# Optimization experiments

Hardware: AMD Instinct MI355X
Metric: run time of the kernel (lower is better)

The kernel has to match this reference:

```python
import jax, jax.numpy as jnp
import numpy as np

N, G, HID, LAT, E_RAND = 20000, 3000, 256, 32, 320000
EPS = 1e-8
NEG_SLOPE = 0.2  # PyG GATv2Conv default leaky_relu slope


def _segment_softmax(logits, seg, n):
    # numerically stable softmax over edges grouped by destination node
    m = jax.ops.segment_max(logits, seg, num_segments=n)
    ex = jnp.exp(logits - m[seg])
    s = jax.ops.segment_sum(ex, seg, num_segments=n)
    return ex / (s[seg] + 1e-16)


def _gatv2(x, src, dst, Wl, Wr, att, b, n):
    # GATv2 (heads=1): score = att . leaky_relu(Wl x_j + Wr x_i)
    xl = x @ Wl  # [N, C] source transform (also the message)
    xr = x @ Wr  # [N, C] destination transform
    e = jax.nn.leaky_relu(xl[src] + xr[dst], NEG_SLOPE)  # [E, C]
    logit = e @ att  # [E]
    alpha = _segment_softmax(logit, dst, n)
    out = jax.ops.segment_sum(alpha[:, None] * xl[src], dst, num_segments=n)
    return out + b


def _log_zinb(x, mu, theta, pi):
    theta = theta[None, :]
    softplus_pi = jax.nn.softplus(-pi)
    log_theta_eps = jnp.log(theta + EPS)
    log_theta_mu_eps = jnp.log(theta + mu + EPS)
    pi_theta_log = -pi + theta * (log_theta_eps - log_theta_mu_eps)
    case_zero = jax.nn.softplus(pi_theta_log) - softplus_pi
    case_nz = (-softplus_pi + pi_theta_log
               + x * (jnp.log(mu + EPS) - log_theta_mu_eps)
               + jax.lax.lgamma(x + theta) - jax.lax.lgamma(theta)
               - jax.lax.lgamma(x + 1.0))
    return jnp.where(x < EPS, case_zero, 0.0) + jnp.where(x > EPS, case_nz, 0.0)


def setup_inputs():
    key = jax.random.key(0)
    ks = jax.random.split(key, 14)
    x = jax.random.randint(ks[0], (N, G), 0, 20).astype(jnp.float32)
    er = jax.random.randint(ks[1], (2, E_RAND), 0, N, dtype=jnp.int32)
    loops = jnp.tile(jnp.arange(N, dtype=jnp.int32)[None, :], (2, 1))
    edge_index = jnp.concatenate([er, loops], axis=1)  # [2, 340000] incl self-loops
    noise = jax.random.normal(ks[2], (N, LAT), dtype=jnp.float32)

    def init(k, shape, fan_in):
        return jax.random.normal(k, shape, dtype=jnp.float32) / np.float32(np.sqrt(fan_in))

    Wl1 = init(ks[3], (G, HID), G); Wr1 = init(ks[4], (G, HID), G)
    att1 = init(ks[5], (HID,), HID); b1 = jnp.zeros((HID,), jnp.float32)
    Wl2 = init(ks[6], (HID, 2 * LAT), HID); Wr2 = init(ks[7], (HID, 2 * LAT), HID)
    att2 = init(ks[8], (2 * LAT,), 2 * LAT); b2 = jnp.zeros((2 * LAT,), jnp.float32)
    Wd1 = init(ks[9], (LAT, HID), LAT); bd1 = jnp.zeros((HID,), jnp.float32)
    Wd2 = init(ks[10], (HID, G), HID); bd2 = jnp.zeros((G,), jnp.float32)
    Wdo = init(ks[11], (HID, G), HID); bdo = jnp.zeros((G,), jnp.float32)
    theta = jax.random.uniform(ks[12], (G,), minval=0.5, maxval=2.0, dtype=jnp.float32)
    return dict(x=x, edge_index=edge_index, noise=noise,
                Wl1=Wl1, Wr1=Wr1, att1=att1, b1=b1,
                Wl2=Wl2, Wr2=Wr2, att2=att2, b2=b2,
                Wd1=Wd1, bd1=bd1, Wd2=Wd2, bd2=bd2, Wdo=Wdo, bdo=bdo,
                theta=theta)


def reference(x, edge_index, noise, Wl1, Wr1, att1, b1, Wl2, Wr2, att2, b2,
              Wd1, bd1, Wd2, bd2, Wdo, bdo, theta):
    n = x.shape[0]
    src, dst = edge_index[0], edge_index[1]
    # --- GATv2 encoder ---
    h = _gatv2(x, src, dst, Wl1, Wr1, att1, b1, n)
    h2 = _gatv2(jax.nn.relu(h), src, dst, Wl2, Wr2, att2, b2, n)  # [N, 2*LAT]
    mu_z, logvar = h2[:, :LAT], h2[:, LAT:]
    # --- reparameterize: std = sqrt(exp(logvar)) ---
    z = mu_z + noise * jnp.exp(0.5 * logvar)
    # --- ZINB decoder ---
    hd = z @ Wd1 + bd1
    mean = jax.nn.softplus(hd @ Wd2 + bd2)
    pi = hd @ Wdo + bdo
    # --- loss: -E[log ZINB] + KL(q(z|x) || N(0,I)) ---
    recon = -jnp.mean(jnp.sum(_log_zinb(x, mean, theta, pi), axis=1))
    kl = jnp.mean(0.5 * jnp.sum(mu_z ** 2 + jnp.exp(logvar) - logvar - 1.0, axis=1))
    return recon + kl
```

## Files before the change

kernel.cpp:

```cpp
#include <hip/hip_runtime.h>
#include <math.h>

#define NN   20000
#define GG   3000
#define HIDD 256
#define LATT 32
#define FEPS 1e-8f

typedef __attribute__((ext_vector_type(8))) __bf16 bf16x8;
typedef __attribute__((ext_vector_type(4))) float f32x4;

__device__ __forceinline__ float fsp(float v) {
    float t = __expf(-fabsf(v));
    return fmaxf(v, 0.f) + __logf(1.f + t);
}
__device__ __forceinline__ float sp_approx(float t) {
    float a = fabsf(t);
    float den = fmaf(a, fmaf(a, fmaf(a, 0.8382f, -1.4958f), 1.87f), 1.f);
    return fmaxf(t, 0.f) + 0.6931472f * __builtin_amdgcn_rcpf(den);
}
__device__ __forceinline__ float lrelu(float v) {
    return v > 0.f ? v : 0.2f * v;
}
__device__ __forceinline__ ushort f2bf(float f) {
    uint b = __float_as_uint(f);
    return (ushort)((b + 0x7FFFu + ((b >> 16) & 1u)) >> 16);
}

__global__ void zinb_table(const float* __restrict__ theta, float* __restrict__ tabL,
                           float* __restrict__ logte, int G_) {
    int idx = blockIdx.x * blockDim.x + threadIdx.x;
    if (idx >= G_ * 20) return;
    int g = idx / 20, c = idx % 20;
    float th = theta[g];
    tabL[idx] = lgammaf((float)c + th) - lgammaf(th) - lgammaf((float)c + 1.f);
    if (c == 0) logte[g] = logf(th + FEPS);
}

__global__ void edge_hist(const int* __restrict__ ei, int* __restrict__ cnt, int E) {
    int e = blockIdx.x * blockDim.x + threadIdx.x;
    if (e < E) atomicAdd(&cnt[ei[E + e]], 1);
}

__global__ __launch_bounds__(1024)
void scan_deg(int* __restrict__ cnt_cur, int* __restrict__ rowptr, int Nn) {
    __shared__ int ts[1024];
    int t = threadIdx.x;
    int chunk = (Nn + 1023) / 1024;
    int beg = t * chunk, end = min(beg + chunk, Nn);
    int s = 0;
    for (int i = beg; i < end; i++) s += cnt_cur[i];
    ts[t] = s;
    __syncthreads();
    for (int off = 1; off < 1024; off <<= 1) {
        int v = (t >= off) ? ts[t - off] : 0;
        __syncthreads();
        ts[t] += v;
        __syncthreads();
    }
    int run = (t == 0) ? 0 : ts[t - 1];
    for (int i = beg; i < end; i++) {
        int c = cnt_cur[i];
        rowptr[i] = run;
        cnt_cur[i] = run;
        run += c;
    }
    if (t == 1023) rowptr[Nn] = ts[1023];
}

__global__ void edge_scatter(const int* __restrict__ ei, int* __restrict__ cur,
                             int* __restrict__ eidx, int E) {
    int e = blockIdx.x * blockDim.x + threadIdx.x;
    if (e < E) {
        int p = atomicAdd(&cur[ei[E + e]], 1);
        eidx[p] = e;
    }
}

__global__ __launch_bounds__(256)
void transp_bf16(const float* __restrict__ in, ushort* __restrict__ out, int K, int N) {
    __shared__ ushort t[32][33];
    int k0 = blockIdx.x * 32, n0 = blockIdx.y * 32;
    int tx = threadIdx.x & 31, ty = threadIdx.x >> 5;
    #pragma unroll
    for (int u = 0; u < 32; u += 8) {
        int k = k0 + ty + u, n = n0 + tx;
        t[ty + u][tx] = (k < K && n < N) ? f2bf(in[(size_t)k * N + n]) : (ushort)0;
    }
    __syncthreads();
    #pragma unroll
    for (int u = 0; u < 32; u += 8) {
        int n = n0 + ty + u, k = k0 + tx;
        if (n < N && k < K) out[(size_t)n * K + k] = t[tx][ty + u];
    }
}

template<bool ABF, bool ZEP>
__global__ __launch_bounds__(256, 4)
void mfma_dual(const void* __restrict__ Ap, const ushort* __restrict__ B1t,
               const ushort* __restrict__ B2t, float* __restrict__ C1,
               float* __restrict__ C2, const float* __restrict__ xg,
               const float* __restrict__ tabL, const float* __restrict__ theta,
               const float* __restrict__ logte, const float* __restrict__ bd2,
               const float* __restrict__ bdo, double* __restrict__ partsR,
               int M, int K, int Nc) {
    __shared__ __align__(16) char lds[ZEP ? 32768 : 24576];
    char* ldsA  = lds;
    char* ldsB1 = lds + 8192;
    char* ldsB2 = lds + 16384;
    char* xsb   = lds + 24576;
    __shared__ float thetas[ZEP ? 64 : 1], thltes[ZEP ? 64 : 1];
    __shared__ float bd2s[ZEP ? 64 : 1], bdos[ZEP ? 64 : 1];
    __shared__ float tabs[ZEP ? 64 * 20 : 1];
    __shared__ double redd[4];

    const int tid = threadIdx.x;
    const int nwg = gridDim.x * gridDim.y;
    const int orig = blockIdx.y * gridDim.x + blockIdx.x;
    const int q = nwg >> 3, r = nwg & 7, xcd = orig & 7;
    const int vv = (xcd < r ? xcd * (q + 1) : r * (q + 1) + (xcd - r) * q) + (orig >> 3);
    const int bx = vv % gridDim.x, by = vv / gridDim.x;
    const int m0 = by * 64, n0 = bx * 64;
    const int lane = tid & 63, wid = tid >> 6;
    const int wr = wid >> 1, wc = wid & 1;
    const int frow = lane & 15;
    const int fkb = (lane >> 4) << 4;

    if (ZEP) {
        #pragma unroll
        for (int u = 0; u < 2; u++) {
            int c = tid + (u << 8);
            int row = c >> 3, col8 = (c & 7) << 3;
            int gm = m0 + row, gn = n0 + col8;
            uint4 w = make_uint4(0u, 0u, 0u, 0u);
            if (gm < M && gn < Nc) {
                const float* af = xg + (size_t)gm * Nc + gn;
                float4 lo = *(const float4*)af;
                float4 hi = *(const float4*)(af + 4);
                w.x = (uint)f2bf(lo.x) | ((uint)f2bf(lo.y) << 16);
                w.y = (uint)f2bf(lo.z) | ((uint)f2bf(lo.w) << 16);
                w.z = (uint)f2bf(hi.x) | ((uint)f2bf(hi.y) << 16);
                w.w = (uint)f2bf(hi.z) | ((uint)f2bf(hi.w) << 16);
            }
            int o = (row << 7) + (col8 << 1);
            o ^= (row & 7) << 4;
            *(uint4*)(xsb + o) = w;
        }
        for (int i = tid; i < 64; i += 256) {
            int g = n0 + i;
            bool ok = g < Nc;
            float th = ok ? theta[g] : 1.f;
            thetas[i] = th;
            thltes[i] = ok ? th * logte[g] : 0.f;
            bd2s[i]   = ok ? bd2[g]   : 0.f;
            bdos[i]   = ok ? bdo[g]   : 0.f;
        }
        for (int i = tid; i < 64 * 20; i += 256) {
            int g = n0 + i / 20;
            tabs[i] = (g < Nc) ? tabL[(size_t)g * 20 + i % 20] : 0.f;
        }
    }

    f32x4 acc1[2][2], acc2[2][2];
    #pragma unroll
    for (int i = 0; i < 2; i++)
        #pragma unroll
        for (int j = 0; j < 2; j++) {
            acc1[i][j] = (f32x4){0.f, 0.f, 0.f, 0.f};
            acc2[i][j] = (f32x4){0.f, 0.f, 0.f, 0.f};
        }

    const int nk = (K + 63) >> 6;
    for (int t = 0; t < nk; t++) {
        const int k0 = t << 6;
        #pragma unroll
        for (int u = 0; u < 2; u++) {
            int c = tid + (u << 8);
            int row = c >> 3, col8 = (c & 7) << 3;
            int gm = m0 + row, gk = k0 + col8;
            uint4 w = make_uint4(0u, 0u, 0u, 0u);
            if (gm < M && gk < K) {
                if (ABF) {
                    w = *(const uint4*)((const ushort*)Ap + (size_t)gm * K + gk);
                } else {
                    const float* af = (const float*)Ap + (size_t)gm * K + gk;
                    float4 lo = *(const float4*)af;
                    float4 hi = *(const float4*)(af + 4);
                    w.x = (uint)f2bf(lo.x) | ((uint)f2bf(lo.y) << 16);
                    w.y = (uint)f2bf(lo.z) | ((uint)f2bf(lo.w) << 16);
                    w.z = (uint)f2bf(hi.x) | ((uint)f2bf(hi.y) << 16);
                    w.w = (uint)f2bf(hi.z) | ((uint)f2bf(hi.w) << 16);
                }
            }
            int o = (row << 7) + (col8 << 1);
            o ^= (row & 7) << 4;
            *(uint4*)(ldsA + o) = w;
        }
        #pragma unroll
        for (int u = 0; u < 2; u++) {
            int c = tid + (u << 8);
            int row = c >> 3, col8 = (c & 7) << 3;
            int gn = n0 + row, gk = k0 + col8;
            uint4 w1 = make_uint4(0u, 0u, 0u, 0u), w2 = w1;
            if (gn < Nc && gk < K) {
                size_t o = (size_t)gn * K + gk;
                w1 = *(const uint4*)(B1t + o);
                w2 = *(const uint4*)(B2t + o);
            }
            int o = (row << 7) + (col8 << 1);
            o ^= (row & 7) << 4;
            *(uint4*)(ldsB1 + o) = w1;
            *(uint4*)(ldsB2 + o) = w2;
        }
        __syncthreads();
        #pragma unroll
        for (int kk = 0; kk < 2; kk++) {
            int kb = (kk << 6) + fkb;
            bf16x8 af[2], b1f[2], b2f[2];
            #pragma unroll
            for (int mi = 0; mi < 2; mi++) {
                int rr = (wr << 5) + (mi << 4) + frow;
                int o = ((rr << 7) + kb) ^ ((rr & 7) << 4);
                af[mi] = *(const bf16x8*)(ldsA + o);
            }
            #pragma unroll
            for (int ni = 0; ni < 2; ni++) {
                int rr = (wc << 5) + (ni << 4) + frow;
                int o = ((rr << 7) + kb) ^ ((rr & 7) << 4);
                b1f[ni] = *(const bf16x8*)(ldsB1 + o);
                b2f[ni] = *(const bf16x8*)(ldsB2 + o);
            }
            #pragma unroll
            for (int mi = 0; mi < 2; mi++)
                #pragma unroll
                for (int ni = 0; ni < 2; ni++) {
                    acc1[mi][ni] = __builtin_amdgcn_mfma_f32_16x16x32_bf16(af[mi], b1f[ni], acc1[mi][ni], 0, 0, 0);
                    acc2[mi][ni] = __builtin_amdgcn_mfma_f32_16x16x32_bf16(af[mi], b2f[ni], acc2[mi][ni], 0, 0, 0);
                }
        }
        __syncthreads();
    }

    const int lr = (lane >> 4) << 2;
    if (!ZEP) {
        #pragma unroll
        for (int mi = 0; mi < 2; mi++)
            #pragma unroll
            for (int ni = 0; ni < 2; ni++) {
                int gmb = m0 + (wr << 5) + (mi << 4) + lr;
                int gn  = n0 + (wc << 5) + (ni << 4) + frow;
                if (gn >= Nc) continue;
                f32x4 v1 = acc1[mi][ni], v2 = acc2[mi][ni];
                #pragma unroll
                for (int j = 0; j < 4; j++) {
                    int gm = gmb + j;
                    if (gm < M) {
                        C1[(size_t)gm * Nc + gn] = v1[j];
                        C2[(size_t)gm * Nc + gn] = v2[j];
                    }
                }
            }
    } else {
        float lsum = 0.f;
        #pragma unroll
        for (int mi = 0; mi < 2; mi++)
            #pragma unroll
            for (int ni = 0; ni < 2; ni++) {
                int lcol = (wc << 5) + (ni << 4) + frow;
                int gn = n0 + lcol;
                int lrow0 = (wr << 5) + (mi << 4) + lr;
                if (gn >= Nc) continue;
                f32x4 am = acc1[mi][ni], ap = acc2[mi][ni];
                float th = thetas[lcol], thlte = thltes[lcol];
                float bm = bd2s[lcol], bp = bdos[lcol];
                #pragma unroll
                for (int j = 0; j < 4; j++) {
                    int lrow = lrow0 + j;
                    if (m0 + lrow >= M) continue;
                    float mu  = fsp(am[j] + bm);
                    float pi  = ap[j] + bp;
                    float spp = fsp(pi);
                    float ltme = __logf(th + mu + FEPS);
                    float lmu  = __logf(mu + FEPS);
                    int o = (lrow << 7) + (lcol << 1);
                    o ^= (lrow & 7) << 4;
                    ushort ub = *(const ushort*)(xsb + o);
                    float xv = __uint_as_float((uint)ub << 16);
                    int xi = (int)(xv + 0.5f);
                    float ptl = fmaf(-th, ltme, thlte) - pi;
                    float corr = (xv < FEPS) ? sp_approx(-ptl) : 0.f;
                    float term = thlte + tabs[lcol * 20 + xi] - spp
                               - (th + xv) * ltme + xv * lmu + corr;
                    lsum += term;
                }
            }
        #pragma unroll
        for (int off = 32; off; off >>= 1) lsum += __shfl_down(lsum, off);
        if (lane == 0) redd[wid] = (double)lsum;
        __syncthreads();
        if (tid == 0)
            partsR[by * gridDim.x + bx] = redd[0] + redd[1] + redd[2] + redd[3];
    }
}

template<int DW, int OM>
__global__ __launch_bounds__(256)
void gat_attn(const float* __restrict__ xl, const float* __restrict__ xr,
              const float* __restrict__ att, const int* __restrict__ ei,
              const int* __restrict__ rowptr, const int* __restrict__ eidx,
              const float* __restrict__ bias, void* __restrict__ out,
              int D, int Nn) {
    __shared__ float lbuf[4][64];
    int wid = threadIdx.x >> 6, lane = threadIdx.x & 63;
    int n = blockIdx.x * 4 + wid;
    if (n >= Nn) return;
    int k = lane * DW;
    float xrr[DW], ats[DW], hacc[DW];
    if (DW == 4) {
        float4 a4 = *(const float4*)(att + k);
        float4 r4 = *(const float4*)(xr + (size_t)n * D + k);
        ats[0] = a4.x; ats[1] = a4.y; ats[2] = a4.z; ats[3] = a4.w;
        xrr[0] = r4.x; xrr[1] = r4.y; xrr[2] = r4.z; xrr[3] = r4.w;
    } else {
        ats[0] = att[k];
        xrr[0] = xr[(size_t)n * D + k];
    }
    #pragma unroll
    for (int d = 0; d < DW; d++) hacc[d] = 0.f;
    float m = -3.0e38f, ssum = 0.f;
    int beg = rowptr[n], end = rowptr[n + 1];
    for (int c0 = beg; c0 < end; c0 += 64) {
        int cnt = min(64, end - c0);
        for (int j = 0; j < cnt; j++) {
            int e = eidx[c0 + j];
            const float* xs = xl + (size_t)ei[e] * D + k;
            float p;
            if (DW == 4) {
                float4 v = *(const float4*)xs;
                p = ats[0] * lrelu(v.x + xrr[0]) + ats[1] * lrelu(v.y + xrr[1])
                  + ats[2] * lrelu(v.z + xrr[2]) + ats[3] * lrelu(v.w + xrr[3]);
            } else {
                p = ats[0] * lrelu(xs[0] + xrr[0]);
            }
            #pragma unroll
            for (int o2 = 32; o2; o2 >>= 1) p += __shfl_down(p, o2);
            if (lane == 0) lbuf[wid][j] = p;
        }
        float cm = (lane < cnt) ? lbuf[wid][lane] : -3.0e38f;
        #pragma unroll
        for (int o2 = 32; o2; o2 >>= 1) cm = fmaxf(cm, __shfl_xor(cm, o2));
        float mnew = fmaxf(m, cm);
        float scale = __expf(m - mnew);
        ssum *= scale;
        #pragma unroll
        for (int d = 0; d < DW; d++) hacc[d] *= scale;
        for (int j = 0; j < cnt; j++) {
            int e = eidx[c0 + j];
            float w = __expf(lbuf[wid][j] - mnew);
            ssum += w;
            const float* xs = xl + (size_t)ei[e] * D + k;
            if (DW == 4) {
                float4 v = *(const float4*)xs;
                hacc[0] = fmaf(w, v.x, hacc[0]);
                hacc[1] = fmaf(w, v.y, hacc[1]);
                hacc[2] = fmaf(w, v.z, hacc[2]);
                hacc[3] = fmaf(w, v.w, hacc[3]);
            } else {
                hacc[0] = fmaf(w, xs[0], hacc[0]);
            }
        }
        m = mnew;
    }
    float inv = 1.f / (ssum + 1e-16f);
    if (DW == 4) {
        float4 b = *(const float4*)(bias + k);
        float r0 = fmaf(hacc[0], inv, b.x), r1 = fmaf(hacc[1], inv, b.y);
        float r2 = fmaf(hacc[2], inv, b.z), r3 = fmaf(hacc[3], inv, b.w);
        if (OM == 0) {
            *(float4*)((float*)out + (size_t)n * D + k) = make_float4(r0, r1, r2, r3);
        } else {
            ushort4 o;
            o.x = f2bf(fmaxf(r0, 0.f)); o.y = f2bf(fmaxf(r1, 0.f));
            o.z = f2bf(fmaxf(r2, 0.f)); o.w = f2bf(fmaxf(r3, 0.f));
            *(ushort4*)((ushort*)out + (size_t)n * D + k) = o;
        }
    } else {
        float r0 = fmaf(hacc[0], inv, bias[k]);
        if (OM == 0) ((float*)out)[(size_t)n * D + k] = r0;
        else         ((ushort*)out)[(size_t)n * D + k] = f2bf(fmaxf(r0, 0.f));
    }
}

__global__ __launch_bounds__(256)
void z_kl(const float* __restrict__ h2, const float* __restrict__ noise,
          float* __restrict__ z, double* __restrict__ partsK, int Nn) {
    __shared__ double rd[4];
    int gid = blockIdx.x * blockDim.x + threadIdx.x;
    int n = gid >> 5, k = gid & 31;
    float kt = 0.f;
    if (n < Nn) {
        float mu = h2[(size_t)n * 64 + k];
        float lv = h2[(size_t)n * 64 + 32 + k];
        float ev = expf(lv);
        z[(size_t)n * 32 + k] = mu + noise[(size_t)n * 32 + k] * expf(0.5f * lv);
        kt = 0.5f * (mu * mu + ev - lv - 1.f);
    }
    #pragma unroll
    for (int off = 32; off; off >>= 1) kt += __shfl_down(kt, off);
    int wid = threadIdx.x >> 6, lane = threadIdx.x & 63;
    if (lane == 0) rd[wid] = (double)kt;
    __syncthreads();
    if (threadIdx.x == 0) partsK[blockIdx.x] = rd[0] + rd[1] + rd[2] + rd[3];
}

__global__ __launch_bounds__(256)
void hd_gemm(const float* __restrict__ z, const float* __restrict__ Wd1,
             const float* __restrict__ bd1, ushort* __restrict__ hd, int Nn) {
    __shared__ float Ws[32 * 256];
    __shared__ float zs[32 * 32];
    int tid = threadIdx.x;
    #pragma unroll
    for (int i = 0; i < 32; i++) Ws[i * 256 + tid] = Wd1[i * 256 + tid];
    int r0 = blockIdx.x * 32;
    for (int i = tid; i < 32 * 32; i += 256) {
        int r = i >> 5, c = i & 31;
        zs[i] = (r0 + r < Nn) ? z[(size_t)(r0 + r) * 32 + c] : 0.f;
    }
    __syncthreads();
    float b = bd1[tid];
    for (int r = 0; r < 32; r++) {
        if (r0 + r >= Nn) break;
        float acc = b;
        #pragma unroll
        for (int k2 = 0; k2 < 32; k2++) acc = fmaf(zs[r * 32 + k2], Ws[k2 * 256 + tid], acc);
        hd[(size_t)(r0 + r) * 256 + tid] = f2bf(acc);
    }
}

__global__ __launch_bounds__(256)
void final_reduce(const double* __restrict__ pR, int nR,
                  const double* __restrict__ pK, int nK,
                  float* __restrict__ out, int Nn) {
    __shared__ double sd[256];
    double s = 0.0;
    for (int i = threadIdx.x; i < nR; i += 256) s -= pR[i];
    for (int i = threadIdx.x; i < nK; i += 256) s += pK[i];
    sd[threadIdx.x] = s;
    __syncthreads();
    for (int o = 128; o; o >>= 1) {
        if (threadIdx.x < o) sd[threadIdx.x] += sd[threadIdx.x + o];
        __syncthreads();
    }
    if (threadIdx.x == 0) out[0] = (float)(sd[0] / (double)Nn);
}

extern "C" void kernel_launch(void* const* d_in, const int* in_sizes, int n_in,
                              void* d_out, int out_size, void* d_ws, size_t ws_size,
                              hipStream_t stream) {
    const int N_ = NN, G_ = GG, HID_ = HIDD;
    const float* x     = (const float*)d_in[0];
    const int*   ei    = (const int*)d_in[1];
    const float* noise = (const float*)d_in[2];
    const float* Wl1   = (const float*)d_in[3];
    const float* Wr1   = (const float*)d_in[4];
    const float* att1  = (const float*)d_in[5];
    const float* b1    = (const float*)d_in[6];
    const float* Wl2   = (const float*)d_in[7];
    const float* Wr2   = (const float*)d_in[8];
    const float* att2  = (const float*)d_in[9];
    const float* b2    = (const float*)d_in[10];
    const float* Wd1   = (const float*)d_in[11];
    const float* bd1   = (const float*)d_in[12];
    const float* Wd2   = (const float*)d_in[13];
    const float* bd2   = (const float*)d_in[14];
    const float* Wdo   = (const float*)d_in[15];
    const float* bdo   = (const float*)d_in[16];
    const float* theta = (const float*)d_in[17];
    const int E = in_sizes[1] / 2;

    const int MB = (N_ + 63) / 64;
    const int dgx = (G_ + 63) / 64;
    const int nR = dgx * MB;
    const int nKb = (N_ * 32) / 256;

    char* base = (char*)d_ws;
    size_t off = 0;
    auto alloc = [&](size_t bytes) -> char* {
        char* p = base + off;
        off = (off + bytes + 255) & ~(size_t)255;
        return p;
    };
    double* partsR = (double*)alloc((size_t)nR * 8);
    double* partsK = (double*)alloc((size_t)nKb * 8);
    float*  tabL  = (float*)alloc((size_t)G_ * 20 * 4);
    float*  logte = (float*)alloc((size_t)G_ * 4);
    int*    rowptr= (int*)alloc((size_t)(N_ + 1) * 4);
    int*    cur   = (int*)alloc((size_t)N_ * 4);
    int*    eidx  = (int*)alloc((size_t)E * 4);
    ushort* Wl1t  = (ushort*)alloc((size_t)HID_ * G_ * 2);
    ushort* Wr1t  = (ushort*)alloc((size_t)HID_ * G_ * 2);
    ushort* Wl2t  = (ushort*)alloc((size_t)64 * HID_ * 2);
    ushort* Wr2t  = (ushort*)alloc((size_t)64 * HID_ * 2);
    ushort* Wd2t  = (ushort*)alloc((size_t)G_ * HID_ * 2);
    ushort* Wdot  = (ushort*)alloc((size_t)G_ * HID_ * 2);
    float*  xl1   = (float*)alloc((size_t)N_ * HID_ * 4);
    float*  xr1   = (float*)alloc((size_t)N_ * HID_ * 4);
    ushort* h_bf  = (ushort*)alloc((size_t)N_ * HID_ * 2);
    float*  xl2   = (float*)alloc((size_t)N_ * 64 * 4);
    float*  xr2   = (float*)alloc((size_t)N_ * 64 * 4);
    float*  h2    = (float*)alloc((size_t)N_ * 64 * 4);
    float*  zb    = (float*)alloc((size_t)N_ * 32 * 4);

    ushort* hdb = (ushort*)xr1;
    float*  outf = (float*)d_out;

    hipMemsetAsync(cur, 0, N_ * sizeof(int), stream);

    zinb_table<<<(G_ * 20 + 255) / 256, 256, 0, stream>>>(theta, tabL, logte, G_);
    edge_hist<<<(E + 255) / 256, 256, 0, stream>>>(ei, cur, E);
    scan_deg<<<1, 1024, 0, stream>>>(cur, rowptr, N_);
    edge_scatter<<<(E + 255) / 256, 256, 0, stream>>>(ei, cur, eidx, E);

    transp_bf16<<<dim3((G_ + 31) / 32, (HID_ + 31) / 32), 256, 0, stream>>>(Wl1, Wl1t, G_, HID_);
    transp_bf16<<<dim3((G_ + 31) / 32, (HID_ + 31) / 32), 256, 0, stream>>>(Wr1, Wr1t, G_, HID_);
    transp_bf16<<<dim3((HID_ + 31) / 32, 2), 256, 0, stream>>>(Wl2, Wl2t, HID_, 64);
    transp_bf16<<<dim3((HID_ + 31) / 32, 2), 256, 0, stream>>>(Wr2, Wr2t, HID_, 64);
    transp_bf16<<<dim3((HID_ + 31) / 32, (G_ + 31) / 32), 256, 0, stream>>>(Wd2, Wd2t, HID_, G_);
    transp_bf16<<<dim3((HID_ + 31) / 32, (G_ + 31) / 32), 256, 0, stream>>>(Wdo, Wdot, HID_, G_);

    mfma_dual<false, false><<<dim3(HID_ / 64, MB), 256, 0, stream>>>(
        x, Wl1t, Wr1t, xl1, xr1, nullptr, nullptr, nullptr, nullptr, nullptr, nullptr, nullptr,
        N_, G_, HID_);
    gat_attn<4, 1><<<(N_ + 3) / 4, 256, 0, stream>>>(
        xl1, xr1, att1, ei, rowptr, eidx, b1, h_bf, HID_, N_);

    mfma_dual<true, false><<<dim3(1, MB), 256, 0, stream>>>(
        h_bf, Wl2t, Wr2t, xl2, xr2, nullptr, nullptr, nullptr, nullptr, nullptr, nullptr, nullptr,
        N_, HID_, 64);
    gat_attn<1, 0><<<(N_ + 3) / 4, 256, 0, stream>>>(
        xl2, xr2, att2, ei, rowptr, eidx, b2, h2, 64, N_);

    z_kl<<<nKb, 256, 0, stream>>>(h2, noise, zb, partsK, N_);

    hd_gemm<<<(N_ + 31) / 32, 256, 0, stream>>>(zb, Wd1, bd1, hdb, N_);
    mfma_dual<true, true><<<dim3(dgx, MB), 256, 0, stream>>>(
        hdb, Wd2t, Wdot, nullptr, nullptr, x, tabL, theta, logte, bd2, bdo, partsR,
        N_, HID_, G_);

    final_reduce<<<1, 256, 0, stream>>>(partsR, nR, partsK, nKb, outf, N_);
}
```

Baseline: 750.5 us.

## Use 128x128 tiled GEMM with direct global-to-LDS loads for large GEMMs

Adds a new gemm_big kernel with 512 threads and 128x128 output tiles, used for the first encoder GEMM and the fused ZINB decoder GEMM. B tiles (and A when bf16) are loaded with global_load_lds directly into swizzled LDS, and the transposed Wl1/Wr1 are padded to K=3008 so the K loop has no bounds checks. The ZINB epilogue now reads x straight from global memory instead of staging a bf16 copy in LDS. Larger tiles raise reuse per loaded byte and cut the number of blocks. The cost is higher register and LDS use per block, and fewer blocks across the CUs.

Result: faster. 687.9 us (-8.3%).

```diff
diff --git a/kernel.cpp b/kernel.cpp
--- a/kernel.cpp
+++ b/kernel.cpp
@@ -25,6 +25,13 @@
 __device__ __forceinline__ ushort f2bf(float f) {
     uint b = __float_as_uint(f);
     return (ushort)((b + 0x7FFFu + ((b >> 16) & 1u)) >> 16);
+}
+__device__ __forceinline__ uint pk2(float a, float b) {
+    return (uint)f2bf(a) | ((uint)f2bf(b) << 16);
+}
+__device__ __forceinline__ void gload16(const void* g, void* l) {
+    __builtin_amdgcn_global_load_lds((const __attribute__((address_space(1))) void*)g,
+                                     (__attribute__((address_space(3))) void*)l, 16, 0, 0);
 }
 
 __global__ void zinb_table(const float* __restrict__ theta, float* __restrict__ tabL,
@@ -78,7 +85,8 @@
 }
 
 __global__ __launch_bounds__(256)
-void transp_bf16(const float* __restrict__ in, ushort* __restrict__ out, int K, int N) {
+void transp_bf16(const float* __restrict__ in, ushort* __restrict__ out,
+                 int K, int N, int Kpad) {
     __shared__ ushort t[32][33];
     int k0 = blockIdx.x * 32, n0 = blockIdx.y * 32;
     int tx = threadIdx.x & 31, ty = threadIdx.x >> 5;
@@ -91,28 +99,27 @@
     #pragma unroll
     for (int u = 0; u < 32; u += 8) {
         int n = n0 + ty + u, k = k0 + tx;
-        if (n < N && k < K) out[(size_t)n * K + k] = t[tx][ty + u];
+        if (n < N && k < Kpad) out[(size_t)n * Kpad + k] = t[tx][ty + u];
     }
 }
 
 template<bool ABF, bool ZEP>
-__global__ __launch_bounds__(256, 4)
-void mfma_dual(const void* __restrict__ Ap, const ushort* __restrict__ B1t,
-               const ushort* __restrict__ B2t, float* __restrict__ C1,
-               float* __restrict__ C2, const float* __restrict__ xg,
-               const float* __restrict__ tabL, const float* __restrict__ theta,
-               const float* __restrict__ logte, const float* __restrict__ bd2,
-               const float* __restrict__ bdo, double* __restrict__ partsR,
-               int M, int K, int Nc) {
-    __shared__ __align__(16) char lds[ZEP ? 32768 : 24576];
+__global__ __launch_bounds__(512, 4)
+void gemm_big(const void* __restrict__ Ap, const ushort* __restrict__ B1t,
+              const ushort* __restrict__ B2t, float* __restrict__ C1,
+              float* __restrict__ C2, const float* __restrict__ xg,
+              const float* __restrict__ tabL, const float* __restrict__ theta,
+              const float* __restrict__ logte, const float* __restrict__ bd2,
+              const float* __restrict__ bdo, double* __restrict__ partsR,
+              int M, int Kreal, int Kpad, int Nc) {
+    __shared__ __align__(16) char lds[49152];
     char* ldsA  = lds;
-    char* ldsB1 = lds + 8192;
-    char* ldsB2 = lds + 16384;
-    char* xsb   = lds + 24576;
-    __shared__ float thetas[ZEP ? 64 : 1], thltes[ZEP ? 64 : 1];
-    __shared__ float bd2s[ZEP ? 64 : 1], bdos[ZEP ? 64 : 1];
-    __shared__ float tabs[ZEP ? 64 * 20 : 1];
-    __shared__ double redd[4];
+    char* ldsB1 = lds + 16384;
+    char* ldsB2 = lds + 32768;
+    __shared__ float tabs[ZEP ? 128 * 20 : 1];
+    __shared__ float thetas[ZEP ? 128 : 1], thltes[ZEP ? 128 : 1];
+    __shared__ float bd2s[ZEP ? 128 : 1], bdos[ZEP ? 128 : 1];
+    __shared__ double redd[8];
 
     const int tid = threadIdx.x;
     const int nwg = gridDim.x * gridDim.y;
@@ -120,106 +127,104 @@
     const int q = nwg >> 3, r = nwg & 7, xcd = orig & 7;
     const int vv = (xcd < r ? xcd * (q + 1) : r * (q + 1) + (xcd - r) * q) + (orig >> 3);
     const int bx = vv % gridDim.x, by = vv / gridDim.x;
-    const int m0 = by * 64, n0 = bx * 64;
+    const int m0 = by * 128, n0 = bx * 128;
     const int lane = tid & 63, wid = tid >> 6;
-    const int wr = wid >> 1, wc = wid & 1;
+    const int wr = wid >> 2, wc = wid & 3;
     const int frow = lane & 15;
     const int fkb = (lane >> 4) << 4;
 
     if (ZEP) {
-        #pragma unroll
-        for (int u = 0; u < 2; u++) {
-            int c = tid + (u << 8);
-            int row = c >> 3, col8 = (c & 7) << 3;
-            int gm = m0 + row, gn = n0 + col8;
-            uint4 w = make_uint4(0u, 0u, 0u, 0u);
-            if (gm < M && gn < Nc) {
-                const float* af = xg + (size_t)gm * Nc + gn;
-                float4 lo = *(const float4*)af;
-                float4 hi = *(const float4*)(af + 4);
-                w.x = (uint)f2bf(lo.x) | ((uint)f2bf(lo.y) << 16);
-                w.y = (uint)f2bf(lo.z) | ((uint)f2bf(lo.w) << 16);
-                w.z = (uint)f2bf(hi.x) | ((uint)f2bf(hi.y) << 16);
-                w.w = (uint)f2bf(hi.z) | ((uint)f2bf(hi.w) << 16);
-            }
-            int o = (row << 7) + (col8 << 1);
-            o ^= (row & 7) << 4;
-            *(uint4*)(xsb + o) = w;
-        }
-        for (int i = tid; i < 64; i += 256) {
+        for (int i = tid; i < 128; i += 512) {
             int g = n0 + i;
             bool ok = g < Nc;
             float th = ok ? theta[g] : 1.f;
             thetas[i] = th;
             thltes[i] = ok ? th * logte[g] : 0.f;
-            bd2s[i]   = ok ? bd2[g]   : 0.f;
-            bdos[i]   = ok ? bdo[g]   : 0.f;
-        }
-        for (int i = tid; i < 64 * 20; i += 256) {
+            bd2s[i]   = ok ? bd2[g] : 0.f;
+            bdos[i]   = ok ? bdo[g] : 0.f;
+        }
+        for (int i = tid; i < 128 * 20; i += 512) {
             int g = n0 + i / 20;
             tabs[i] = (g < Nc) ? tabL[(size_t)g * 20 + i % 20] : 0.f;
         }
     }
 
-    f32x4 acc1[2][2], acc2[2][2];
-    #pragma unroll
-    for (int i = 0; i < 2; i++)
+    f32x4 acc1[4][2], acc2[4][2];
+    #pragma unroll
+    for (int i = 0; i < 4; i++)
         #pragma unroll
         for (int j = 0; j < 2; j++) {
             acc1[i][j] = (f32x4){0.f, 0.f, 0.f, 0.f};
             acc2[i][j] = (f32x4){0.f, 0.f, 0.f, 0.f};
         }
 
-    const int nk = (K + 63) >> 6;
+    const int row_in = lane >> 3;
+    const int sch = (lane & 7) ^ (row_in & 7);
+    const int ldso = (lane << 4);
+
+    const int nk = Kpad >> 6;
     for (int t = 0; t < nk; t++) {
         const int k0 = t << 6;
         #pragma unroll
         for (int u = 0; u < 2; u++) {
-            int c = tid + (u << 8);
-            int row = c >> 3, col8 = (c & 7) << 3;
-            int gm = m0 + row, gk = k0 + col8;
-            uint4 w = make_uint4(0u, 0u, 0u, 0u);
-            if (gm < M && gk < K) {
-                if (ABF) {
-                    w = *(const uint4*)((const ushort*)Ap + (size_t)gm * K + gk);
+            int s = (wid << 1) + u;
+            int grow = n0 + (s << 3) + row_in;
+            if (grow > Nc - 1) grow = Nc - 1;
+            size_t go = (size_t)grow * Kpad + k0 + (sch << 3);
+            gload16(B1t + go, ldsB1 + (s << 10) + ldso);
+            gload16(B2t + go, ldsB2 + (s << 10) + ldso);
+        }
+        if (ABF) {
+            #pragma unroll
+            for (int u = 0; u < 2; u++) {
+                int s = (wid << 1) + u;
+                int grow = m0 + (s << 3) + row_in;
+                if (grow > M - 1) grow = M - 1;
+                size_t go = (size_t)grow * Kpad + k0 + (sch << 3);
+                gload16((const ushort*)Ap + go, ldsA + (s << 10) + ldso);
+            }
+        } else {
+            int arow = tid >> 2;
+            int acol = (tid & 3) << 4;
+            int gm = m0 + arow;
+            uint4 w0 = make_uint4(0u, 0u, 0u, 0u), w1 = w0;
+            if (gm < M) {
+                const float* af = (const float*)Ap + (size_t)gm * Kreal + k0 + acol;
+                if (k0 + 64 <= Kreal) {
+                    float4 a = ((const float4*)af)[0];
+                    float4 b = ((const float4*)af)[1];
+                    float4 c = ((const float4*)af)[2];
+                    float4 d = ((const float4*)af)[3];
+                    w0.x = pk2(a.x, a.y); w0.y = pk2(a.z, a.w);
+                    w0.z = pk2(b.x, b.y); w0.w = pk2(b.z, b.w);
+                    w1.x = pk2(c.x, c.y); w1.y = pk2(c.z, c.w);
+                    w1.z = pk2(d.x, d.y); w1.w = pk2(d.z, d.w);
                 } else {
-                    const float* af = (const float*)Ap + (size_t)gm * K + gk;
-                    float4 lo = *(const float4*)af;
-                    float4 hi = *(const float4*)(af + 4);
-                    w.x = (uint)f2bf(lo.x) | ((uint)f2bf(lo.y) << 16);
-                    w.y = (uint)f2bf(lo.z) | ((uint)f2bf(lo.w) << 16);
-                    w.z = (uint)f2bf(hi.x) | ((uint)f2bf(hi.y) << 16);
-                    w.w = (uint)f2bf(hi.z) | ((uint)f2bf(hi.w) << 16);
+                    float tmp[16];
+                    #pragma unroll
+                    for (int jj = 0; jj < 16; jj++) {
+                        int gk = k0 + acol + jj;
+                        tmp[jj] = (gk < Kreal) ? af[jj] : 0.f;
+                    }
+                    w0.x = pk2(tmp[0], tmp[1]);  w0.y = pk2(tmp[2], tmp[3]);
+                    w0.z = pk2(tmp[4], tmp[5]);  w0.w = pk2(tmp[6], tmp[7]);
+                    w1.x = pk2(tmp[8], tmp[9]);  w1.y = pk2(tmp[10], tmp[11]);
+                    w1.z = pk2(tmp[12], tmp[13]); w1.w = pk2(tmp[14], tmp[15]);
                 }
             }
-            int o = (row << 7) + (col8 << 1);
-            o ^= (row & 7) << 4;
-            *(uint4*)(ldsA + o) = w;
-        }
-        #pragma unroll
-        for (int u = 0; u < 2; u++) {
-            int c = tid + (u << 8);
-            int row = c >> 3, col8 = (c & 7) << 3;
-            int gn = n0 + row, gk = k0 + col8;
-            uint4 w1 = make_uint4(0u, 0u, 0u, 0u), w2 = w1;
-            if (gn < Nc && gk < K) {
-                size_t o = (size_t)gn * K + gk;
-                w1 = *(const uint4*)(B1t + o);
-                w2 = *(const uint4*)(B2t + o);
-            }
-            int o = (row << 7) + (col8 << 1);
-            o ^= (row & 7) << 4;
-            *(uint4*)(ldsB1 + o) = w1;
-            *(uint4*)(ldsB2 + o) = w2;
+            int o0 = ((arow << 7) + (acol << 1)) ^ ((arow & 7) << 4);
+            int o1 = ((arow << 7) + ((acol + 8) << 1)) ^ ((arow & 7) << 4);
+            *(uint4*)(ldsA + o0) = w0;
+            *(uint4*)(ldsA + o1) = w1;
         }
         __syncthreads();
         #pragma unroll
         for (int kk = 0; kk < 2; kk++) {
             int kb = (kk << 6) + fkb;
-            bf16x8 af[2], b1f[2], b2f[2];
-            #pragma unroll
-            for (int mi = 0; mi < 2; mi++) {
-                int rr = (wr << 5) + (mi << 4) + frow;
+            bf16x8 af[4], b1f[2], b2f[2];
+            #pragma unroll
+            for (int mi = 0; mi < 4; mi++) {
+                int rr = (wr << 6) + (mi << 4) + frow;
                 int o = ((rr << 7) + kb) ^ ((rr & 7) << 4);
                 af[mi] = *(const bf16x8*)(ldsA + o);
             }
@@ -231,7 +236,7 @@
                 b2f[ni] = *(const bf16x8*)(ldsB2 + o);
             }
             #pragma unroll
-            for (int mi = 0; mi < 2; mi++)
+            for (int mi = 0; mi < 4; mi++)
                 #pragma unroll
                 for (int ni = 0; ni < 2; ni++) {
                     acc1[mi][ni] = __builtin_amdgcn_mfma_f32_16x16x32_bf16(af[mi], b1f[ni], acc1[mi][ni], 0, 0, 0);
@@ -244,10 +249,10 @@
     const int lr = (lane >> 4) << 2;
     if (!ZEP) {
         #pragma unroll
-        for (int mi = 0; mi < 2; mi++)
+        for (int mi = 0; mi < 4; mi++)
             #pragma unroll
             for (int ni = 0; ni < 2; ni++) {
-                int gmb = m0 + (wr << 5) + (mi << 4) + lr;
+                int gmb = m0 + (wr << 6) + (mi << 4) + lr;
                 int gn  = n0 + (wc << 5) + (ni << 4) + frow;
                 if (gn >= Nc) continue;
                 f32x4 v1 = acc1[mi][ni], v2 = acc2[mi][ni];
@@ -263,44 +268,148 @@
     } else {
         float lsum = 0.f;
         #pragma unroll
-        for (int mi = 0; mi < 2; mi++)
+        for (int mi = 0; mi < 4; mi++)
             #pragma unroll
             for (int ni = 0; ni < 2; ni++) {
                 int lcol = (wc << 5) + (ni << 4) + frow;
                 int gn = n0 + lcol;
-                int lrow0 = (wr << 5) + (mi << 4) + lr;
+                int lrow0 = (wr << 6) + (mi << 4) + lr;
                 if (gn >= Nc) continue;
                 f32x4 am = acc1[mi][ni], ap = acc2[mi][ni];
                 float th = thetas[lcol], thlte = thltes[lcol];
                 float bm = bd2s[lcol], bp = bdos[lcol];
                 #pragma unroll
                 for (int j = 0; j < 4; j++) {
-                    int lrow = lrow0 + j;
-                    if (m0 + lrow >= M) continue;
+                    int gm = m0 + lrow0 + j;
+                    if (gm >= M) continue;
                     float mu  = fsp(am[j] + bm);
                     float pi  = ap[j] + bp;
                     float spp = fsp(pi);
                     float ltme = __logf(th + mu + FEPS);
                     float lmu  = __logf(mu + FEPS);
-                    int o = (lrow << 7) + (lcol << 1);
-                    o ^= (lrow & 7) << 4;
-                    ushort ub = *(const ushort*)(xsb + o);
-                    float xv = __uint_as_float((uint)ub << 16);
+                    float xv = xg[(size_t)gm * Nc + gn];
                     int xi = (int)(xv + 0.5f);
                     float ptl = fmaf(-th, ltme, thlte) - pi;
                     float corr = (xv < FEPS) ? sp_approx(-ptl) : 0.f;
-                    float term = thlte + tabs[lcol * 20 + xi] - spp
-                               - (th + xv) * ltme + xv * lmu + corr;
-                    lsum += term;
+                    lsum += thlte + tabs[lcol * 20 + xi] - spp
+                          - (th + xv) * ltme + xv * lmu + corr;
                 }
             }
         #pragma unroll
         for (int off = 32; off; off >>= 1) lsum += __shfl_down(lsum, off);
         if (lane == 0) redd[wid] = (double)lsum;
         __syncthreads();
-        if (tid == 0)
-            partsR[by * gridDim.x + bx] = redd[0] + redd[1] + redd[2] + redd[3];
-    }
+        if (tid == 0) {
+            double s = 0.0;
+            #pragma unroll
+            for (int i = 0; i < 8; i++) s += redd[i];
+            partsR[by * gridDim.x + bx] = s;
+        }
+    }
+}
+
+template<bool ABF, bool ZEP>
+__global__ __launch_bounds__(256, 4)
+void mfma_dual(const void* __restrict__ Ap, const ushort* __restrict__ B1t,
+               const ushort* __restrict__ B2t, float* __restrict__ C1,
+               float* __restrict__ C2, int M, int K, int Nc) {
+    __shared__ __align__(16) char lds[24576];
+    char* ldsA  = lds;
+    char* ldsB1 = lds + 8192;
+    char* ldsB2 = lds + 16384;
+
+    const int tid = threadIdx.x;
+    const int m0 = blockIdx.y * 64, n0 = blockIdx.x * 64;
+    const int lane = tid & 63, wid = tid >> 6;
+    const int wr = wid >> 1, wc = wid & 1;
+    const int frow = lane & 15;
+    const int fkb = (lane >> 4) << 4;
+
+    f32x4 acc1[2][2], acc2[2][2];
+    #pragma unroll
+    for (int i = 0; i < 2; i++)
+        #pragma unroll
+        for (int j = 0; j < 2; j++) {
+            acc1[i][j] = (f32x4){0.f, 0.f, 0.f, 0.f};
+            acc2[i][j] = (f32x4){0.f, 0.f, 0.f, 0.f};
+        }
+
+    const int nk = (K + 63) >> 6;
+    for (int t = 0; t < nk; t++) {
+        const int k0 = t << 6;
+        #pragma unroll
+        for (int u = 0; u < 2; u++) {
+            int c = tid + (u << 8);
+            int row = c >> 3, col8 = (c & 7) << 3;
+            int gm = m0 + row, gk = k0 + col8;
+            uint4 w = make_uint4(0u, 0u, 0u, 0u);
+            if (gm < M && gk < K)
+                w = *(const uint4*)((const ushort*)Ap + (size_t)gm * K + gk);
+            int o = ((row << 7) + (col8 << 1)) ^ ((row & 7) << 4);
+            *(uint4*)(ldsA + o) = w;
+        }
+        #pragma unroll
+        for (int u = 0; u < 2; u++) {
+            int c = tid + (u << 8);
+            int row = c >> 3, col8 = (c & 7) << 3;
+            int gn = n0 + row, gk = k0 + col8;
+            uint4 w1 = make_uint4(0u, 0u, 0u, 0u), w2 = w1;
+            if (gn < Nc && gk < K) {
+                size_t o = (size_t)gn * K + gk;
+                w1 = *(const uint4*)(B1t + o);
+                w2 = *(const uint4*)(B2t + o);
+            }
+            int o = ((row << 7) + (col8 << 1)) ^ ((row & 7) << 4);
+            *(uint4*)(ldsB1 + o) = w1;
+            *(uint4*)(ldsB2 + o) = w2;
+        }
+        __syncthreads();
+        #pragma unroll
+        for (int kk = 0; kk < 2; kk++) {
+            int kb = (kk << 6) + fkb;
+            bf16x8 af[2], b1f[2], b2f[2];
+            #pragma unroll
+            for (int mi = 0; mi < 2; mi++) {
+                int rr = (wr << 5) + (mi << 4) + frow;
+                int o = ((rr << 7) + kb) ^ ((rr & 7) << 4);
+                af[mi] = *(const bf16x8*)(ldsA + o);
+            }
+            #pragma unroll
+            for (int ni = 0; ni < 2; ni++) {
+                int rr = (wc << 5) + (ni << 4) + frow;
+                int o = ((rr << 7) + kb) ^ ((rr & 7) << 4);
+                b1f[ni] = *(const bf16x8*)(ldsB1 + o);
+                b2f[ni] = *(const bf16x8*)(ldsB2 + o);
+            }
+            #pragma unroll
+            for (int mi = 0; mi < 2; mi++)
+                #pragma unroll
+                for (int ni = 0; ni < 2; ni++) {
+                    acc1[mi][ni] = __builtin_amdgcn_mfma_f32_16x16x32_bf16(af[mi], b1f[ni], acc1[mi][ni], 0, 0, 0);
+                    acc2[mi][ni] = __builtin_amdgcn_mfma_f32_16x16x32_bf16(af[mi], b2f[ni], acc2[mi][ni], 0, 0, 0);
+                }
+        }
+        __syncthreads();
+    }
+
+    const int lr = (lane >> 4) << 2;
+    #pragma unroll
+    for (int mi = 0; mi < 2; mi++)
+        #pragma unroll
+        for (int ni = 0; ni < 2; ni++) {
+            int gmb = m0 + (wr << 5) + (mi << 4) + lr;
+            int gn  = n0 + (wc << 5) + (ni << 4) + frow;
+            if (gn >= Nc) continue;
+            f32x4 v1 = acc1[mi][ni], v2 = acc2[mi][ni];
+            #pragma unroll
+            for (int j = 0; j < 4; j++) {
+                int gm = gmb + j;
+                if (gm < M) {
+                    C1[(size_t)gm * Nc + gn] = v1[j];
+                    C2[(size_t)gm * Nc + gn] = v2[j];
+                }
+            }
+        }
 }
 
 template<int DW, int OM>
@@ -458,6 +567,7 @@
                               void* d_out, int out_size, void* d_ws, size_t ws_size,
                               hipStream_t stream) {
     const int N_ = NN, G_ = GG, HID_ = HIDD;
+    const int KP1 = 3008;
     const float* x     = (const float*)d_in[0];
     const int*   ei    = (const int*)d_in[1];
     const float* noise = (const float*)d_in[2];
@@ -478,10 +588,10 @@
     const float* theta = (const float*)d_in[17];
     const int E = in_sizes[1] / 2;
 
-    const int MB = (N_ + 63) / 64;
-    const int dgx = (G_ + 63) / 64;
-    const int nR = dgx * MB;
-    const int nKb = (N_ * 32) / 256;
+    const int MB128 = (N_ + 127) / 128;
+    const int DGX   = (G_ + 127) / 128;
+    const int nR    = DGX * MB128;
+    const int nKb   = (N_ * 32) / 256;
 
     char* base = (char*)d_ws;
     size_t off = 0;
@@ -497,8 +607,8 @@
     int*    rowptr= (int*)alloc((size_t)(N_ + 1) * 4);
     int*    cur   = (int*)alloc((size_t)N_ * 4);
     int*    eidx  = (int*)alloc((size_t)E * 4);
-    ushort* Wl1t  = (ushort*)alloc((size_t)HID_ * G_ * 2);
-    ushort* Wr1t  = (ushort*)alloc((size_t)HID_ * G_ * 2);
+    ushort* Wl1t  = (ushort*)alloc((size_t)HID_ * KP1 * 2);
+    ushort* Wr1t  = (ushort*)alloc((size_t)HID_ * KP1 * 2);
     ushort* Wl2t  = (ushort*)alloc((size_t)64 * HID_ * 2);
     ushort* Wr2t  = (ushort*)alloc((size_t)64 * HID_ * 2);
     ushort* Wd2t  = (ushort*)alloc((size_t)G_ * HID_ * 2);
@@ -521,31 +631,30 @@
     scan_deg<<<1, 1024, 0, stream>>>(cur, rowptr, N_);
     edge_scatter<<<(E + 255) / 256, 256, 0, stream>>>(ei, cur, eidx, E);
 
-    transp_bf16<<<dim3((G_ + 31) / 32, (HID_ + 31) / 32), 256, 0, stream>>>(Wl1, Wl1t, G_, HID_);
-    transp_bf16<<<dim3((G_ + 31) / 32, (HID_ + 31) / 32), 256, 0, stream>>>(Wr1, Wr1t, G_, HID_);
-    transp_bf16<<<dim3((HID_ + 31) / 32, 2), 256, 0, stream>>>(Wl2, Wl2t, HID_, 64);
-    transp_bf16<<<dim3((HID_ + 31) / 32, 2), 256, 0, stream>>>(Wr2, Wr2t, HID_, 64);
-    transp_bf16<<<dim3((HID_ + 31) / 32, (G_ + 31) / 32), 256, 0, stream>>>(Wd2, Wd2t, HID_, G_);
-    transp_bf16<<<dim3((HID_ + 31) / 32, (G_ + 31) / 32), 256, 0, stream>>>(Wdo, Wdot, HID_, G_);
-
-    mfma_dual<false, false><<<dim3(HID_ / 64, MB), 256, 0, stream>>>(
+    transp_bf16<<<dim3(KP1 / 32, (HID_ + 31) / 32), 256, 0, stream>>>(Wl1, Wl1t, G_, HID_, KP1);
+    transp_bf16<<<dim3(KP1 / 32, (HID_ + 31) / 32), 256, 0, stream>>>(Wr1, Wr1t, G_, HID_, KP1);
+    transp_bf16<<<dim3(HID_ / 32, 2), 256, 0, stream>>>(Wl2, Wl2t, HID_, 64, HID_);
+    transp_bf16<<<dim3(HID_ / 32, (G_ + 31) / 32), 256, 0, stream>>>(Wd2, Wd2t, HID_, G_, HID_);
+    transp_bf16<<<dim3(HID_ / 32, (G_ + 31) / 32), 256, 0, stream>>>(Wdo, Wdot, HID_, G_, HID_);
+    transp_bf16<<<dim3(HID_ / 32, 2), 256, 0, stream>>>(Wr2, Wr2t, HID_, 64, HID_);
+
+    gemm_big<false, false><<<dim3(HID_ / 128, MB128), 512, 0, stream>>>(
         x, Wl1t, Wr1t, xl1, xr1, nullptr, nullptr, nullptr, nullptr, nullptr, nullptr, nullptr,
-        N_, G_, HID_);
+        N_, G_, KP1, HID_);
     gat_attn<4, 1><<<(N_ + 3) / 4, 256, 0, stream>>>(
         xl1, xr1, att1, ei, rowptr, eidx, b1, h_bf, HID_, N_);
 
-    mfma_dual<true, false><<<dim3(1, MB), 256, 0, stream>>>(
-        h_bf, Wl2t, Wr2t, xl2, xr2, nullptr, nullptr, nullptr, nullptr, nullptr, nullptr, nullptr,
-        N_, HID_, 64);
+    mfma_dual<true, false><<<dim3(1, (N_ + 63) / 64), 256, 0, stream>>>(
+        h_bf, Wl2t, Wr2t, xl2, xr2, N_, HID_, 64);
     gat_attn<1, 0><<<(N_ + 3) / 4, 256, 0, stream>>>(
         xl2, xr2, att2, ei, rowptr, eidx, b2, h2, 64, N_);
 
     z_kl<<<nKb, 256, 0, stream>>>(h2, noise, zb, partsK, N_);
 
     hd_gemm<<<(N_ + 31) / 32, 256, 0, stream>>>(zb, Wd1, bd1, hdb, N_);
-    mfma_dual<true, true><<<dim3(dgx, MB), 256, 0, stream>>>(
+    gemm_big<true, true><<<dim3(DGX, MB128), 512, 0, stream>>>(
         hdb, Wd2t, Wdot, nullptr, nullptr, x, tabL, theta, logte, bd2, bdo, partsR,
-        N_, HID_, G_);
+        N_, HID_, HID_, G_);
 
     final_reduce<<<1, 256, 0, stream>>>(partsR, nR, partsK, nKb, outf, N_);
 }
```
